# Kernel optimization log

Hardware: AMD Instinct MI355X
Metric: run time of the kernel (lower is better)

The kernel has to match this reference:

```python
import jax, jax.numpy as jnp
import numpy as np

B, S, IN_F, OUT_F = 8, 2048, 2048, 2048
ORDER, RANK, LEAF = 3, 4, 13  # LEAF = ceil(IN_F ** (1/ORDER))


def setup_inputs() -> dict:
    key = jax.random.key(0)
    k1, k2, k3, k4 = jax.random.split(key, 4)
    inp = jax.random.normal(k1, (B, S, IN_F), dtype=jnp.float32)
    # leaf init ~ uniform(-std, std), std = gain / in_features**(1/order)
    gain = float(np.sqrt(2.0 / (1.0 + 5.0)))  # leaky_relu gain with param=sqrt(5)
    std = gain / (IN_F ** (1.0 / ORDER))
    leaf_tensor = jax.random.uniform(k2, (ORDER, RANK, LEAF, LEAF), dtype=jnp.float32,
                                     minval=-std, maxval=std)
    bound = 1.0 / np.sqrt(IN_F)
    weight = jax.random.uniform(k3, (OUT_F, IN_F), dtype=jnp.float32, minval=-bound, maxval=bound)
    bias = jax.random.uniform(k4, (OUT_F,), dtype=jnp.float32, minval=-bound, maxval=bound)
    return {"input": inp, "leaf_tensor": leaf_tensor, "weight": weight, "bias": bias}


def tensor_product_represent(leaf_tensor, out_dim, in_dim):
    order, rank, leaf, _ = leaf_tensor.shape  # static shapes
    base = leaf_tensor[0]                      # [rank, leaf, leaf]
    dim = leaf
    for i in range(1, order):                  # fixed small structural loop
        # Kronecker step: [r, d, d] x [r, l, l] -> [r, d*l, d*l]
        base = jnp.einsum('abc,ade->abdce', base, leaf_tensor[i])
        dim = dim * leaf
        base = base.reshape(rank, dim, dim)
    base = base.sum(axis=0)                    # [leaf^order, leaf^order]
    return base[:out_dim, :in_dim]


def reference(input, leaf_tensor, weight, bias):
    out_dim, in_dim = weight.shape
    delta = tensor_product_represent(leaf_tensor, out_dim, in_dim)
    w = weight + delta                          # [out, in]
    # F.linear: y = x @ w.T + b
    return jnp.einsum('bsi,oi->bso', input, w) + bias
```

## Files before the change

kernel.cpp:

```cpp
#include <hip/hip_runtime.h>
#include <hip/hip_bf16.h>
#include <stdint.h>

#define MROWS 16384
#define KDIM  2048
#define NDIM  2048
#define LEAFD 13
#define RANKD 4

typedef __bf16 bf16x8 __attribute__((ext_vector_type(8)));
typedef float  f32x4  __attribute__((ext_vector_type(4)));

__global__ void build_w_kernel(const float* __restrict__ weight,
                               const float* __restrict__ leaf,
                               __hip_bfloat16* __restrict__ wbf) {
    __shared__ float ll[3 * RANKD * LEAFD * LEAFD];
    for (int t = threadIdx.x; t < 3 * RANKD * LEAFD * LEAFD; t += blockDim.x)
        ll[t] = leaf[t];
    __syncthreads();
    int idx = blockIdx.x * blockDim.x + threadIdx.x;
    if (idx >= NDIM * KDIM) return;
    int o = idx / KDIM, i = idx % KDIM;
    int o2 = o / 169, o1 = (o / 13) % 13, o0 = o % 13;
    int i2 = i / 169, i1 = (i / 13) % 13, i0 = i % 13;
    float d = 0.f;
#pragma unroll
    for (int r = 0; r < RANKD; ++r) {
        float a = ll[( r            * LEAFD + o2) * LEAFD + i2];
        float b = ll[((RANKD   + r) * LEAFD + o1) * LEAFD + i1];
        float c = ll[((2*RANKD + r) * LEAFD + o0) * LEAFD + i0];
        d += a * b * c;
    }
    wbf[idx] = __float2bfloat16(weight[idx] + d);
}

__global__ void cvt_kernel(const float* __restrict__ x,
                           __hip_bfloat16* __restrict__ xb, int n) {
    long stride = (long)gridDim.x * blockDim.x * 4;
    for (long idx = ((long)blockIdx.x * blockDim.x + threadIdx.x) * 4; idx < n; idx += stride) {
        float4 v = *reinterpret_cast<const float4*>(x + idx);
        __hip_bfloat16 tmp[4];
        tmp[0] = __float2bfloat16(v.x);
        tmp[1] = __float2bfloat16(v.y);
        tmp[2] = __float2bfloat16(v.z);
        tmp[3] = __float2bfloat16(v.w);
        *reinterpret_cast<uint2*>(xb + idx) = *reinterpret_cast<const uint2*>(tmp);
    }
}


__device__ __forceinline__ void gload16(const __hip_bfloat16* g, char* l) {
    __builtin_amdgcn_global_load_lds((const __attribute__((address_space(1))) void*)g,
                                     (__attribute__((address_space(3))) void*)l,
                                     16, 0, 0);
}

#define STAGE(base, kb, bufi, slot) do {                                          \
    gload16((base) + (kb) + gOff0, smemc + (bufi)*65536 + (slot)*16384 + lOff0);  \
    gload16((base) + (kb) + gOff1, smemc + (bufi)*65536 + (slot)*16384 + lOff1);  \
} while (0)

#define LOAD_A(mh, kk, bufc)                                                        \
    af0 = *(const bf16x8*)(smemc + (bufc)*65536 + (kk)*32768 + offA[(mh)*4+0]);     \
    af1 = *(const bf16x8*)(smemc + (bufc)*65536 + (kk)*32768 + offA[(mh)*4+1]);     \
    af2 = *(const bf16x8*)(smemc + (bufc)*65536 + (kk)*32768 + offA[(mh)*4+2]);     \
    af3 = *(const bf16x8*)(smemc + (bufc)*65536 + (kk)*32768 + offA[(mh)*4+3]);

#define LOAD_B(kk, bufc)                                                                    \
    bf0 = *(const bf16x8*)(smemc + (bufc)*65536 + (kk)*32768 + 16384 + offB[0]);            \
    bf1 = *(const bf16x8*)(smemc + (bufc)*65536 + (kk)*32768 + 16384 + offB[1]);            \
    bf2 = *(const bf16x8*)(smemc + (bufc)*65536 + (kk)*32768 + 16384 + offB[2]);            \
    bf3 = *(const bf16x8*)(smemc + (bufc)*65536 + (kk)*32768 + 16384 + offB[3]);

#define MFMA_Q(mh) do {                                                                   \
    acc[(mh)*4+0][0] = __builtin_amdgcn_mfma_f32_16x16x32_bf16(af0, bf0, acc[(mh)*4+0][0], 0,0,0); \
    acc[(mh)*4+1][0] = __builtin_amdgcn_mfma_f32_16x16x32_bf16(af1, bf0, acc[(mh)*4+1][0], 0,0,0); \
    acc[(mh)*4+2][0] = __builtin_amdgcn_mfma_f32_16x16x32_bf16(af2, bf0, acc[(mh)*4+2][0], 0,0,0); \
    acc[(mh)*4+3][0] = __builtin_amdgcn_mfma_f32_16x16x32_bf16(af3, bf0, acc[(mh)*4+3][0], 0,0,0); \
    acc[(mh)*4+0][1] = __builtin_amdgcn_mfma_f32_16x16x32_bf16(af0, bf1, acc[(mh)*4+0][1], 0,0,0); \
    acc[(mh)*4+1][1] = __builtin_amdgcn_mfma_f32_16x16x32_bf16(af1, bf1, acc[(mh)*4+1][1], 0,0,0); \
    acc[(mh)*4+2][1] = __builtin_amdgcn_mfma_f32_16x16x32_bf16(af2, bf1, acc[(mh)*4+2][1], 0,0,0); \
    acc[(mh)*4+3][1] = __builtin_amdgcn_mfma_f32_16x16x32_bf16(af3, bf1, acc[(mh)*4+3][1], 0,0,0); \
    acc[(mh)*4+0][2] = __builtin_amdgcn_mfma_f32_16x16x32_bf16(af0, bf2, acc[(mh)*4+0][2], 0,0,0); \
    acc[(mh)*4+1][2] = __builtin_amdgcn_mfma_f32_16x16x32_bf16(af1, bf2, acc[(mh)*4+1][2], 0,0,0); \
    acc[(mh)*4+2][2] = __builtin_amdgcn_mfma_f32_16x16x32_bf16(af2, bf2, acc[(mh)*4+2][2], 0,0,0); \
    acc[(mh)*4+3][2] = __builtin_amdgcn_mfma_f32_16x16x32_bf16(af3, bf2, acc[(mh)*4+3][2], 0,0,0); \
    acc[(mh)*4+0][3] = __builtin_amdgcn_mfma_f32_16x16x32_bf16(af0, bf3, acc[(mh)*4+0][3], 0,0,0); \
    acc[(mh)*4+1][3] = __builtin_amdgcn_mfma_f32_16x16x32_bf16(af1, bf3, acc[(mh)*4+1][3], 0,0,0); \
    acc[(mh)*4+2][3] = __builtin_amdgcn_mfma_f32_16x16x32_bf16(af2, bf3, acc[(mh)*4+2][3], 0,0,0); \
    acc[(mh)*4+3][3] = __builtin_amdgcn_mfma_f32_16x16x32_bf16(af3, bf3, acc[(mh)*4+3][3], 0,0,0); \
} while (0)

#define BARRIER_IN do {                                     \
    __builtin_amdgcn_sched_barrier(0);                      \
    __builtin_amdgcn_s_barrier();                           \
    asm volatile("s_waitcnt lgkmcnt(0)" ::: "memory");      \
    __builtin_amdgcn_sched_barrier(0);                      \
    __builtin_amdgcn_s_setprio(1);                          \
} while (0)

#define BARRIER_OUT do {                                    \
    __builtin_amdgcn_s_setprio(0);                          \
    __builtin_amdgcn_sched_barrier(0);                      \
    __builtin_amdgcn_s_barrier();                           \
    __builtin_amdgcn_sched_barrier(0);                      \
} while (0)

#define WAIT4 asm volatile("s_waitcnt vmcnt(4)" ::: "memory")
#define WAIT0 asm volatile("s_waitcnt vmcnt(0)" ::: "memory")
#define WNONE do {} while (0)

#define KTILE(t, bufc, S0, S1, S2, S3, W3) do {                     \
                                                  \
    LOAD_B(0, bufc); LOAD_A(0, 0, bufc);                            \
    if (S0) STAGE(Abase, ((t)+1)*64+32, (bufc)^1, 2);               \
    BARRIER_IN; MFMA_Q(0); BARRIER_OUT;                             \
                                                  \
    LOAD_A(1, 0, bufc);                                             \
    if (S1) STAGE(Bbase, ((t)+1)*64+32, (bufc)^1, 3);               \
    BARRIER_IN; MFMA_Q(1); BARRIER_OUT;                             \
                                                  \
    LOAD_B(1, bufc); LOAD_A(0, 1, bufc);                            \
    if (S2) STAGE(Abase, ((t)+2)*64, (bufc), 0);                    \
    BARRIER_IN; MFMA_Q(0); BARRIER_OUT;                             \
                                                  \
    LOAD_A(1, 1, bufc);                                             \
    if (S3) STAGE(Bbase, ((t)+2)*64, (bufc), 1);                    \
    W3;                                                             \
    BARRIER_IN; MFMA_Q(1); BARRIER_OUT;                             \
} while (0)

__global__ __launch_bounds__(512, 2) void gemm8_kernel(const __hip_bfloat16* __restrict__ A,
                                                       const __hip_bfloat16* __restrict__ Wb,
                                                       const float* __restrict__ bias,
                                                       float* __restrict__ C) {
    __shared__ __align__(16) __hip_bfloat16 smem[2][4][8192];
    char* smemc = (char*)&smem[0][0][0];

    const int tid  = threadIdx.x;
    const int lane = tid & 63;
    const int wid  = tid >> 6;
    const int wr   = wid >> 2;
    const int wc   = wid & 3;

    const int bid = blockIdx.x;
    const int swz = (bid & 7) * 64 + (bid >> 3);
    const int bn  = swz >> 6;
    const int bm  = swz & 63;

    const __hip_bfloat16* Abase = A  + (size_t)bm * 256 * KDIM;
    const __hip_bfloat16* Bbase = Wb + (size_t)bn * 256 * KDIM;

    const int c0  = wid * 64 + lane;
    const int c1  = 512 + wid * 64 + lane;
    const int cs0 = c0 ^ ((c0 >> 3) & 7);
    const int cs1 = c1 ^ ((c1 >> 3) & 7);
    const int gOff0 = (cs0 >> 2) * KDIM + (cs0 & 3) * 8;
    const int gOff1 = (cs1 >> 2) * KDIM + (cs1 & 3) * 8;
    const int lOff0 = wid * 1024;
    const int lOff1 = 8192 + wid * 1024;

    const int rsel = lane & 15;
    const int kby  = (lane >> 4) * 16;
    int offA[8], offB[4];
#pragma unroll
    for (int m = 0; m < 8; ++m) {
        int a = (wr * 128 + m * 16 + rsel) * 64 + kby;
        offA[m] = a ^ (((a >> 7) & 7) << 4);
    }
#pragma unroll
    for (int n = 0; n < 4; ++n) {
        int a = (wc * 64 + n * 16 + rsel) * 64 + kby;
        offB[n] = a ^ (((a >> 7) & 7) << 4);
    }

    f32x4 acc[8][4];
#pragma unroll
    for (int m = 0; m < 8; ++m)
#pragma unroll
        for (int n = 0; n < 4; ++n)
            acc[m][n] = (f32x4){0.f, 0.f, 0.f, 0.f};

    bf16x8 af0, af1, af2, af3, bf0, bf1, bf2, bf3;

    STAGE(Abase,  0, 0, 0);
    STAGE(Bbase,  0, 0, 1);
    STAGE(Abase, 32, 0, 2);
    STAGE(Bbase, 32, 0, 3);
    STAGE(Abase, 64, 1, 0);
    STAGE(Bbase, 64, 1, 1);
    WAIT4;
    __builtin_amdgcn_sched_barrier(0);
    __builtin_amdgcn_s_barrier();
    __builtin_amdgcn_sched_barrier(0);

    for (int tt = 0; tt < 30; tt += 2) {
        KTILE(tt,     0, 1, 1, 1, 1, WAIT4);
        KTILE(tt + 1, 1, 1, 1, 1, 1, WAIT4);
    }
    KTILE(30, 0, 1, 1, 0, 0, WAIT0);
    KTILE(31, 1, 0, 0, 0, 0, WNONE);

    const int col0 = lane & 15;
    const int r0   = (lane >> 4) * 4;
#pragma unroll
    for (int n = 0; n < 4; ++n) {
        const int cg = bn * 256 + wc * 64 + n * 16 + col0;
        const float bv = bias[cg];
#pragma unroll
        for (int m = 0; m < 8; ++m) {
            const size_t rg = (size_t)bm * 256 + wr * 128 + m * 16 + r0;
#pragma unroll
            for (int r = 0; r < 4; ++r)
                C[(rg + r) * NDIM + cg] = acc[m][n][r] + bv;
        }
    }
}

__global__ void naive_kernel(const float* __restrict__ x,
                             const float* __restrict__ leaf,
                             const float* __restrict__ W,
                             const float* __restrict__ bias,
                             float* __restrict__ out) {
    long idx = (long)blockIdx.x * blockDim.x + threadIdx.x;
    if (idx >= (long)MROWS * NDIM) return;
    int  o = (int)(idx % NDIM);
    long m = idx / NDIM;
    int o2 = o / 169, o1 = (o / 13) % 13, o0 = o % 13;
    float acc = 0.f;
    for (int i = 0; i < KDIM; ++i) {
        int i2 = i / 169, i1 = (i / 13) % 13, i0 = i % 13;
        float d = 0.f;
#pragma unroll
        for (int r = 0; r < RANKD; ++r)
            d += leaf[( r     * LEAFD + o2) * LEAFD + i2]
               * leaf[((4 + r) * LEAFD + o1) * LEAFD + i1]
               * leaf[((8 + r) * LEAFD + o0) * LEAFD + i0];
        acc += x[m * KDIM + i] * (W[(long)o * KDIM + i] + d);
    }
    out[idx] = acc + bias[o];
}

extern "C" void kernel_launch(void* const* d_in, const int* in_sizes, int n_in,
                              void* d_out, int out_size, void* d_ws, size_t ws_size,
                              hipStream_t stream) {
    const float* x      = (const float*)d_in[0];
    const float* leaf   = (const float*)d_in[1];
    const float* weight = (const float*)d_in[2];
    const float* bias   = (const float*)d_in[3];
    float* out = (float*)d_out;

    const size_t needA = (size_t)MROWS * KDIM * sizeof(__hip_bfloat16);
    const size_t needW = (size_t)NDIM  * KDIM * sizeof(__hip_bfloat16);

    if (ws_size >= needA + needW) {
        __hip_bfloat16* xb = (__hip_bfloat16*)d_ws;
        __hip_bfloat16* wb = (__hip_bfloat16*)((char*)d_ws + needA);
        build_w_kernel<<<(NDIM * KDIM + 255) / 256, 256, 0, stream>>>(weight, leaf, wb);
        cvt_kernel<<<2048, 256, 0, stream>>>(x, xb, MROWS * KDIM);
        gemm8_kernel<<<(MROWS / 256) * (NDIM / 256), 512, 0, stream>>>(xb, wb, bias, out);
    } else {
        long total = (long)MROWS * NDIM;
        naive_kernel<<<(int)((total + 255) / 256), 256, 0, stream>>>(x, leaf, weight, bias, out);
    }
}
```

Before: 208.3 us.

## Fuse fp32-to-bf16 input conversion into GEMM A-tile loading

Removes the separate conversion kernel that wrote a bf16 copy of the 16384x2048 input. The GEMM now loads fp32 A directly into registers, converts it, and writes swizzled bf16 into LDS, while B keeps using direct global-to-LDS loads. The pipeline schedule and vmcnt waits are reworked to interleave the register-staged A loads. This saves a full read and write pass over the activations, but each GEMM block now reads twice as many A bytes, and across all N-blocks that is 8 times. It also adds register pressure and VALU conversion work inside the main loop.

```diff
diff --git a/kernel.cpp b/kernel.cpp
--- a/kernel.cpp
+++ b/kernel.cpp
@@ -34,20 +34,6 @@
     wbf[idx] = __float2bfloat16(weight[idx] + d);
 }
 
-__global__ void cvt_kernel(const float* __restrict__ x,
-                           __hip_bfloat16* __restrict__ xb, int n) {
-    long stride = (long)gridDim.x * blockDim.x * 4;
-    for (long idx = ((long)blockIdx.x * blockDim.x + threadIdx.x) * 4; idx < n; idx += stride) {
-        float4 v = *reinterpret_cast<const float4*>(x + idx);
-        __hip_bfloat16 tmp[4];
-        tmp[0] = __float2bfloat16(v.x);
-        tmp[1] = __float2bfloat16(v.y);
-        tmp[2] = __float2bfloat16(v.z);
-        tmp[3] = __float2bfloat16(v.w);
-        *reinterpret_cast<uint2*>(xb + idx) = *reinterpret_cast<const uint2*>(tmp);
-    }
-}
-
 
 __device__ __forceinline__ void gload16(const __hip_bfloat16* g, char* l) {
     __builtin_amdgcn_global_load_lds((const __attribute__((address_space(1))) void*)g,
@@ -55,9 +41,30 @@
                                      16, 0, 0);
 }
 
-#define STAGE(base, kb, bufi, slot) do {                                          \
-    gload16((base) + (kb) + gOff0, smemc + (bufi)*65536 + (slot)*16384 + lOff0);  \
-    gload16((base) + (kb) + gOff1, smemc + (bufi)*65536 + (slot)*16384 + lOff1);  \
+#define BSTAGE(kb, bufi, slot) do {                                               \
+    gload16(Bbase + (kb) + gOffB0, smemc + (bufi)*65536 + (slot)*16384 + lOff0);  \
+    gload16(Bbase + (kb) + gOffB1, smemc + (bufi)*65536 + (slot)*16384 + lOff1);  \
+} while (0)
+
+#define A_ISSUE(S, koff) do {                                                     \
+    S##0 = *(const f32x4*)(Aptr + (koff) + 0);                                    \
+    S##1 = *(const f32x4*)(Aptr + (koff) + 4);                                    \
+    S##2 = *(const f32x4*)(Aptr + (koff) + 8);                                    \
+    S##3 = *(const f32x4*)(Aptr + (koff) + 12);                                   \
+} while (0)
+
+#define A_WRITE(S, bufi, slot) do {                                               \
+    __hip_bfloat16 wtmp[16];                                                      \
+    wtmp[ 0] = __float2bfloat16(S##0[0]); wtmp[ 1] = __float2bfloat16(S##0[1]);   \
+    wtmp[ 2] = __float2bfloat16(S##0[2]); wtmp[ 3] = __float2bfloat16(S##0[3]);   \
+    wtmp[ 4] = __float2bfloat16(S##1[0]); wtmp[ 5] = __float2bfloat16(S##1[1]);   \
+    wtmp[ 6] = __float2bfloat16(S##1[2]); wtmp[ 7] = __float2bfloat16(S##1[3]);   \
+    wtmp[ 8] = __float2bfloat16(S##2[0]); wtmp[ 9] = __float2bfloat16(S##2[1]);   \
+    wtmp[10] = __float2bfloat16(S##2[2]); wtmp[11] = __float2bfloat16(S##2[3]);   \
+    wtmp[12] = __float2bfloat16(S##3[0]); wtmp[13] = __float2bfloat16(S##3[1]);   \
+    wtmp[14] = __float2bfloat16(S##3[2]); wtmp[15] = __float2bfloat16(S##3[3]);   \
+    *(bf16x8*)(smemc + (bufi)*65536 + (slot)*16384 + aWoff)        = *(bf16x8*)(wtmp);     \
+    *(bf16x8*)(smemc + (bufi)*65536 + (slot)*16384 + (aWoff ^ 16)) = *(bf16x8*)(wtmp + 8); \
 } while (0)
 
 #define LOAD_A(mh, kk, bufc)                                                        \
@@ -106,36 +113,41 @@
     __builtin_amdgcn_sched_barrier(0);                      \
 } while (0)
 
+#define WAIT8 asm volatile("s_waitcnt vmcnt(8)" ::: "memory")
 #define WAIT4 asm volatile("s_waitcnt vmcnt(4)" ::: "memory")
+#define WAIT2 asm volatile("s_waitcnt vmcnt(2)" ::: "memory")
 #define WAIT0 asm volatile("s_waitcnt vmcnt(0)" ::: "memory")
 #define WNONE do {} while (0)
 
-#define KTILE(t, bufc, S0, S1, S2, S3, W3) do {                     \
-                                                  \
-    LOAD_B(0, bufc); LOAD_A(0, 0, bufc);                            \
-    if (S0) STAGE(Abase, ((t)+1)*64+32, (bufc)^1, 2);               \
-    BARRIER_IN; MFMA_Q(0); BARRIER_OUT;                             \
-                                                  \
-    LOAD_A(1, 0, bufc);                                             \
-    if (S1) STAGE(Bbase, ((t)+1)*64+32, (bufc)^1, 3);               \
-    BARRIER_IN; MFMA_Q(1); BARRIER_OUT;                             \
-                                                  \
-    LOAD_B(1, bufc); LOAD_A(0, 1, bufc);                            \
-    if (S2) STAGE(Abase, ((t)+2)*64, (bufc), 0);                    \
-    BARRIER_IN; MFMA_Q(0); BARRIER_OUT;                             \
-                                                  \
-    LOAD_A(1, 1, bufc);                                             \
-    if (S3) STAGE(Bbase, ((t)+2)*64, (bufc), 1);                    \
-    W3;                                                             \
-    BARRIER_IN; MFMA_Q(1); BARRIER_OUT;                             \
-} while (0)
-
-__global__ __launch_bounds__(512, 2) void gemm8_kernel(const __hip_bfloat16* __restrict__ A,
+#define KTILE5(t, bufc, WKHI_, SAKLO_, SBH_, WKLO_, SAKHI_, SBL_, W1_, W3_) do { \
+                                                                         \
+    LOAD_B(0, bufc); LOAD_A(0, 0, bufc);                                         \
+    if (WKHI_)  { A_WRITE(kh, (bufc)^1, 2); }                                    \
+    if (SAKLO_) { A_ISSUE(kl, ((t)+2)*64); }                                     \
+    BARRIER_IN; MFMA_Q(0); BARRIER_OUT;                                          \
+                                                                         \
+    LOAD_A(1, 0, bufc);                                                          \
+    if (SBH_) BSTAGE(((t)+1)*64+32, (bufc)^1, 3);                                \
+    W1_;                                                                         \
+    BARRIER_IN; MFMA_Q(1); BARRIER_OUT;                                          \
+                                                                         \
+    LOAD_B(1, bufc); LOAD_A(0, 1, bufc);                                         \
+    if (WKLO_)  { A_WRITE(kl, (bufc), 0); }                                      \
+    if (SAKHI_) { A_ISSUE(kh, ((t)+2)*64+32); }                                  \
+    BARRIER_IN; MFMA_Q(0); BARRIER_OUT;                                          \
+                                                                         \
+    LOAD_A(1, 1, bufc);                                                          \
+    if (SBL_) BSTAGE(((t)+2)*64, (bufc), 1);                                     \
+    W3_;                                                                         \
+    BARRIER_IN; MFMA_Q(1); BARRIER_OUT;                                          \
+} while (0)
+
+__global__ __launch_bounds__(512, 2) void gemm5_kernel(const float* __restrict__ A32,
                                                        const __hip_bfloat16* __restrict__ Wb,
                                                        const float* __restrict__ bias,
                                                        float* __restrict__ C) {
     __shared__ __align__(16) __hip_bfloat16 smem[2][4][8192];
-    char* smemc = (char*)&smem[0][0][0];
+    char* smemc = (char*)smem;
 
     const int tid  = threadIdx.x;
     const int lane = tid & 63;
@@ -148,15 +160,19 @@
     const int bn  = swz >> 6;
     const int bm  = swz & 63;
 
-    const __hip_bfloat16* Abase = A  + (size_t)bm * 256 * KDIM;
     const __hip_bfloat16* Bbase = Wb + (size_t)bn * 256 * KDIM;
 
+    const int arow = wid * 32 + (lane >> 1);
+    const float* Aptr = A32 + ((size_t)bm * 256 + arow) * KDIM + (lane & 1) * 16;
+    const int p16   = arow * 4 + (lane & 1) * 2;
+    const int aWoff = (p16 ^ ((p16 >> 3) & 7)) * 16;
+
     const int c0  = wid * 64 + lane;
-    const int c1  = 512 + wid * 64 + lane;
+    const int c1  = 512 + c0;
     const int cs0 = c0 ^ ((c0 >> 3) & 7);
     const int cs1 = c1 ^ ((c1 >> 3) & 7);
-    const int gOff0 = (cs0 >> 2) * KDIM + (cs0 & 3) * 8;
-    const int gOff1 = (cs1 >> 2) * KDIM + (cs1 & 3) * 8;
+    const int gOffB0 = (cs0 >> 2) * KDIM + (cs0 & 3) * 8;
+    const int gOffB1 = (cs1 >> 2) * KDIM + (cs1 & 3) * 8;
     const int lOff0 = wid * 1024;
     const int lOff1 = 8192 + wid * 1024;
 
@@ -182,24 +198,30 @@
             acc[m][n] = (f32x4){0.f, 0.f, 0.f, 0.f};
 
     bf16x8 af0, af1, af2, af3, bf0, bf1, bf2, bf3;
-
-    STAGE(Abase,  0, 0, 0);
-    STAGE(Bbase,  0, 0, 1);
-    STAGE(Abase, 32, 0, 2);
-    STAGE(Bbase, 32, 0, 3);
-    STAGE(Abase, 64, 1, 0);
-    STAGE(Bbase, 64, 1, 1);
+    f32x4 kl0, kl1, kl2, kl3;
+    f32x4 kh0, kh1, kh2, kh3;
+
+    A_ISSUE(kl,  0); A_WRITE(kl, 0, 0);
+    A_ISSUE(kl, 32); A_WRITE(kl, 0, 2);
+    A_ISSUE(kl, 64); A_WRITE(kl, 1, 0);
+    A_ISSUE(kl, 96); A_WRITE(kl, 1, 2);
+    BSTAGE( 0, 0, 1);
+    BSTAGE(32, 0, 3);
+    BSTAGE(64, 1, 1);
     WAIT4;
+    asm volatile("s_waitcnt lgkmcnt(0)" ::: "memory");
     __builtin_amdgcn_sched_barrier(0);
     __builtin_amdgcn_s_barrier();
     __builtin_amdgcn_sched_barrier(0);
 
-    for (int tt = 0; tt < 30; tt += 2) {
-        KTILE(tt,     0, 1, 1, 1, 1, WAIT4);
-        KTILE(tt + 1, 1, 1, 1, 1, 1, WAIT4);
-    }
-    KTILE(30, 0, 1, 1, 0, 0, WAIT0);
-    KTILE(31, 1, 0, 0, 0, 0, WNONE);
+    KTILE5(0, 0, 0, 1, 1, 1, 1, 1, WAIT8, WAIT8);
+    for (int t = 1; t < 29; t += 2) {
+        KTILE5(t,     1, 1, 1, 1, 1, 1, 1, WAIT8, WAIT8);
+        KTILE5(t + 1, 0, 1, 1, 1, 1, 1, 1, WAIT8, WAIT8);
+    }
+    KTILE5(29, 1, 1, 1, 1, 1, 1, 1, WAIT8, WAIT8);
+    KTILE5(30, 0, 1, 0, 1, 0, 0, 0, WAIT4, WAIT2);
+    KTILE5(31, 1, 0, 0, 0, 0, 0, 0, WAIT0, WNONE);
 
     const int col0 = lane & 15;
     const int r0   = (lane >> 4) * 4;
@@ -250,15 +272,12 @@
     const float* bias   = (const float*)d_in[3];
     float* out = (float*)d_out;
 
-    const size_t needA = (size_t)MROWS * KDIM * sizeof(__hip_bfloat16);
-    const size_t needW = (size_t)NDIM  * KDIM * sizeof(__hip_bfloat16);
-
-    if (ws_size >= needA + needW) {
-        __hip_bfloat16* xb = (__hip_bfloat16*)d_ws;
-        __hip_bfloat16* wb = (__hip_bfloat16*)((char*)d_ws + needA);
+    const size_t needW = (size_t)NDIM * KDIM * sizeof(__hip_bfloat16);
+
+    if (ws_size >= needW) {
+        __hip_bfloat16* wb = (__hip_bfloat16*)d_ws;
         build_w_kernel<<<(NDIM * KDIM + 255) / 256, 256, 0, stream>>>(weight, leaf, wb);
-        cvt_kernel<<<2048, 256, 0, stream>>>(x, xb, MROWS * KDIM);
-        gemm8_kernel<<<(MROWS / 256) * (NDIM / 256), 512, 0, stream>>>(xb, wb, bias, out);
+        gemm5_kernel<<<(MROWS / 256) * (NDIM / 256), 512, 0, stream>>>(x, wb, bias, out);
     } else {
         long total = (long)MROWS * NDIM;
         naive_kernel<<<(int)((total + 255) / 256), 256, 0, stream>>>(x, leaf, weight, bias, out);
```

New measurement: 232.6 us. 11.7% more time.
